# Kernel tuning notes

Hardware: AMD Instinct MI355X
Metric: run time of the kernel (lower is better)

## Reference

```python
import jax, jax.numpy as jnp
import numpy as np

IN_DIM = 14400
K = 25
DIMS = [7200, 3600, 1800]  # floor(in_dim / 2**(i+1))
OUT_DIM = 2
BATCH = 256


def setup_inputs() -> dict:
    key = jax.random.key(0)
    ks = jax.random.split(key, 32)
    inp = {}
    inp["x"] = jax.random.normal(ks[0], (BATCH, 2 * IN_DIM), dtype=jnp.float32)
    # shared KNN tables (both channels load the same h5 files)
    prev = [IN_DIM] + DIMS[:-1]
    for i, (d, p) in enumerate(zip(DIMS, prev)):
        inp[f"knn{i}"] = jax.random.randint(ks[1 + i], (d, K), 0, p, dtype=jnp.int64)
    std = (2.0 / K) ** 0.5
    kidx = 4
    for ch in ("p", "n"):
        for i, d in enumerate(DIMS):
            inp[f"w{ch}{i}"] = jax.random.normal(ks[kidx], (d, K), dtype=jnp.float32) * std; kidx += 1
            inp[f"b{ch}{i}"] = jnp.zeros((1, d), dtype=jnp.float32)
        inp[f"fc{ch}_w"] = jax.random.normal(ks[kidx], (OUT_DIM, DIMS[-1]), dtype=jnp.float32) * (1.0 / DIMS[-1] ** 0.5); kidx += 1
        inp[f"fc{ch}_b"] = jnp.zeros((OUT_DIM,), dtype=jnp.float32)
    inp["fc3_w"] = jax.random.normal(ks[kidx], (OUT_DIM, 4), dtype=jnp.float32) * 0.5
    inp["fc3_b"] = jnp.zeros((OUT_DIM,), dtype=jnp.float32)
    return inp


def _lcn(x, knns, ws, bs, fw, fb):
    # x: (B, in_dim). Each layer: gather KNN neighbors, weighted sum, bias, relu.
    for knn, w, b in zip(knns, ws, bs):
        g = x[:, knn]                                  # (B, dim, K) gather
        x = jax.nn.relu(jnp.einsum('bdk,dk->bd', g, w) + b)
    return x @ fw.T + fb                               # fc_angle


def reference(x, knn0, knn1, knn2,
              wp0, bp0, wp1, bp1, wp2, bp2, fcp_w, fcp_b,
              wn0, bn0, wn1, bn1, wn2, bn2, fcn_w, fcn_b,
              fc3_w, fc3_b):
    knns = (knn0, knn1, knn2)
    xpos = _lcn(x[:, :IN_DIM], knns, (wp0, wp1, wp2), (bp0, bp1, bp2), fcp_w, fcp_b)
    xneg = _lcn(x[:, IN_DIM:], knns, (wn0, wn1, wn2), (bn0, bn1, bn2), fcn_w, fcn_b)
    h = jax.nn.relu(jnp.concatenate([xpos, xneg], axis=1))  # (B, 4)
    return h @ fc3_w.T + fc3_b
```

## Files before the change

### kernel.cpp

```cpp
#include <hip/hip_runtime.h>
#include <hip/hip_bf16.h>

using bf16 = __hip_bfloat16;

#define K 25
#define B 256

__device__ __forceinline__ float b2f(ushort u) {
  unsigned int w = ((unsigned int)u) << 16;
  float f; __builtin_memcpy(&f, &w, 4); return f;
}
__device__ __forceinline__ ushort f2b(float f) {
  bf16 h = __float2bfloat16(f);
  ushort u; __builtin_memcpy(&u, &h, 2); return u;
}

__device__ __forceinline__ int detect_fdt(const void* x) {
  const unsigned int* xw = (const unsigned int*)x;
  int weird = 0;
  for (int i = 0; i < 64; ++i) {
    unsigned int e = (xw[i * 997] >> 23) & 0xFF;
    weird += (e >= 192) || (e <= 30);
  }
  return (weird >= 32) ? 1 : 0;
}
__device__ __forceinline__ int detect_idt(const void* knn0) {
  const unsigned int* kw = (const unsigned int*)knn0;
  int nz = 0;
  for (int i = 0; i < 64; ++i) nz += (kw[2 * i + 1] != 0);
  return (nz == 0) ? 1 : 0;
}

__global__ __launch_bounds__(256) void transpose_kernel(const void* __restrict__ x,
                                                        const void* __restrict__ knn0,
                                                        ushort* __restrict__ xT,
                                                        float* __restrict__ y,
                                                        int* __restrict__ flags) {
  __shared__ float tile[64][65];
  __shared__ int s_fdt;
  const int t = threadIdx.x;
  if (t == 0) s_fdt = detect_fdt(x);
  __syncthreads();
  const int fdt = s_fdt;

  if (blockIdx.x == 0 && blockIdx.y == 0) {
    if (t == 0) {
      flags[0] = fdt;
      flags[1] = detect_idt(knn0);
      flags[16] = 0;
    }
#pragma unroll
    for (int i = 0; i < 4; ++i) y[t + i * 256] = 0.0f;
  }

  const int f0 = blockIdx.x * 64;
  const int b0 = blockIdx.y * 64;
  if (fdt) {
    const ushort* xp = (const ushort*)x;
#pragma unroll
    for (int q = 0; q < 4; ++q) {
      const int lin = t + q * 256;
      const int bl = lin >> 4;
      const int fq = (lin & 15) << 2;
      const ushort4 v = *(const ushort4*)(xp + (size_t)(b0 + bl) * 28800 + f0 + fq);
      tile[bl][fq] = b2f(v.x); tile[bl][fq + 1] = b2f(v.y);
      tile[bl][fq + 2] = b2f(v.z); tile[bl][fq + 3] = b2f(v.w);
    }
  } else {
    const float* xp = (const float*)x;
#pragma unroll
    for (int q = 0; q < 4; ++q) {
      const int lin = t + q * 256;
      const int bl = lin >> 4;
      const int fq = (lin & 15) << 2;
      const float4 v = *(const float4*)(xp + (size_t)(b0 + bl) * 28800 + f0 + fq);
      tile[bl][fq] = v.x; tile[bl][fq + 1] = v.y;
      tile[bl][fq + 2] = v.z; tile[bl][fq + 3] = v.w;
    }
  }
  __syncthreads();
#pragma unroll
  for (int q = 0; q < 4; ++q) {
    const int lin = t + q * 256;
    const int fl = lin >> 4;
    const int bq = (lin & 15) << 2;
    ushort4 o;
    o.x = f2b(tile[bq][fl]);     o.y = f2b(tile[bq + 1][fl]);
    o.z = f2b(tile[bq + 2][fl]); o.w = f2b(tile[bq + 3][fl]);
    *(ushort4*)(xT + (size_t)(f0 + fl) * B + b0 + bq) = o;
  }
}

__global__ __launch_bounds__(256) void lcn_layer(const ushort* __restrict__ inT,
                                                 const void* __restrict__ knn,
                                                 const void* __restrict__ wp,
                                                 const void* __restrict__ bp,
                                                 const void* __restrict__ wn,
                                                 const void* __restrict__ bn,
                                                 ushort* __restrict__ outT,
                                                 const int* __restrict__ flags,
                                                 int prev, int dout) {
  const int fdt = flags[0];
  const int idt = flags[1];
  const int wave = threadIdx.x >> 6;
  const int lane = threadIdx.x & 63;
  const int d = blockIdx.x * 4 + wave;
  const int ch = blockIdx.y;
  const ushort* in = inT + (size_t)ch * prev * B;
  const void* wsel = ch ? wn : wp;
  const void* bsel = ch ? bn : bp;

  int r[K]; float wk[K];
  if (idt) {
    const long long* ip = (const long long*)knn + (size_t)d * K;
#pragma unroll
    for (int k = 0; k < K; ++k) r[k] = (int)ip[k];
  } else {
    const int* ip = (const int*)knn + (size_t)d * K;
#pragma unroll
    for (int k = 0; k < K; ++k) r[k] = ip[k];
  }
  if (fdt) {
    const ushort* wpp = (const ushort*)wsel + (size_t)d * K;
#pragma unroll
    for (int k = 0; k < K; ++k) wk[k] = b2f(wpp[k]);
  } else {
    const float* wpp = (const float*)wsel + (size_t)d * K;
#pragma unroll
    for (int k = 0; k < K; ++k) wk[k] = wpp[k];
  }
  const float bias = fdt ? b2f(((const ushort*)bsel)[d]) : ((const float*)bsel)[d];

  float a0 = 0.f, a1 = 0.f, a2 = 0.f, a3 = 0.f;
#pragma unroll
  for (int k = 0; k < K; ++k) {
    const ushort4 v = *(const ushort4*)(in + (size_t)r[k] * B + (lane << 2));
    a0 = fmaf(wk[k], b2f(v.x), a0);
    a1 = fmaf(wk[k], b2f(v.y), a1);
    a2 = fmaf(wk[k], b2f(v.z), a2);
    a3 = fmaf(wk[k], b2f(v.w), a3);
  }
  a0 = fmaxf(a0 + bias, 0.f);
  a1 = fmaxf(a1 + bias, 0.f);
  a2 = fmaxf(a2 + bias, 0.f);
  a3 = fmaxf(a3 + bias, 0.f);
  ushort4 o; o.x = f2b(a0); o.y = f2b(a1); o.z = f2b(a2); o.w = f2b(a3);
  *(ushort4*)(outT + ((size_t)ch * dout + d) * B + (lane << 2)) = o;
}

__global__ __launch_bounds__(256) void fc_final_kernel(const ushort* __restrict__ h2,
                                                       const void* __restrict__ fcpw,
                                                       const void* __restrict__ fcnw,
                                                       const void* __restrict__ fcpb,
                                                       const void* __restrict__ fcnb,
                                                       const void* __restrict__ f3w,
                                                       const void* __restrict__ f3b,
                                                       float* __restrict__ y,
                                                       int* __restrict__ flags,
                                                       void* __restrict__ out) {
  const int fdt = flags[0];
  const int wave = threadIdx.x >> 6;
  const int lane = threadIdx.x & 63;
  const int wt = blockIdx.x * 4 + wave;
  __shared__ int s_last;

  if (wt < 450) {
    const int ch = wt >= 225;
    const int c0 = (ch ? wt - 225 : wt) * 8;
    const ushort* h = h2 + (size_t)ch * 1800 * B;
    const void* fw = ch ? fcnw : fcpw;
    float w0[8], w1[8];
    if (fdt) {
      const ushort* fp = (const ushort*)fw;
#pragma unroll
      for (int j = 0; j < 8; ++j) { w0[j] = b2f(fp[c0 + j]); w1[j] = b2f(fp[1800 + c0 + j]); }
    } else {
      const float* fp = (const float*)fw;
#pragma unroll
      for (int j = 0; j < 8; ++j) { w0[j] = fp[c0 + j]; w1[j] = fp[1800 + c0 + j]; }
    }
    float s0[4] = {0.f, 0.f, 0.f, 0.f}, s1[4] = {0.f, 0.f, 0.f, 0.f};
#pragma unroll
    for (int j = 0; j < 8; ++j) {
      const ushort4 v = *(const ushort4*)(h + (size_t)(c0 + j) * B + (lane << 2));
      const float f0v = b2f(v.x), f1v = b2f(v.y), f2v = b2f(v.z), f3v = b2f(v.w);
      s0[0] = fmaf(w0[j], f0v, s0[0]); s0[1] = fmaf(w0[j], f1v, s0[1]);
      s0[2] = fmaf(w0[j], f2v, s0[2]); s0[3] = fmaf(w0[j], f3v, s0[3]);
      s1[0] = fmaf(w1[j], f0v, s1[0]); s1[1] = fmaf(w1[j], f1v, s1[1]);
      s1[2] = fmaf(w1[j], f2v, s1[2]); s1[3] = fmaf(w1[j], f3v, s1[3]);
    }
#pragma unroll
    for (int i = 0; i < 4; ++i) {
      atomicAdd(&y[(ch * 2 + 0) * B + (lane << 2) + i], s0[i]);
      atomicAdd(&y[(ch * 2 + 1) * B + (lane << 2) + i], s1[i]);
    }
  }

  __syncthreads();
  if (threadIdx.x == 0) {
    __threadfence();
    s_last = (atomicAdd(&flags[16], 1) == gridDim.x - 1);
  }
  __syncthreads();
  if (s_last) {
    const int b = threadIdx.x;
    const float y0 = atomicAdd(&y[0 * B + b], 0.0f);
    const float y1 = atomicAdd(&y[1 * B + b], 0.0f);
    const float y2 = atomicAdd(&y[2 * B + b], 0.0f);
    const float y3 = atomicAdd(&y[3 * B + b], 0.0f);
    const float bp0v = fdt ? b2f(((const ushort*)fcpb)[0]) : ((const float*)fcpb)[0];
    const float bp1v = fdt ? b2f(((const ushort*)fcpb)[1]) : ((const float*)fcpb)[1];
    const float bn0v = fdt ? b2f(((const ushort*)fcnb)[0]) : ((const float*)fcnb)[0];
    const float bn1v = fdt ? b2f(((const ushort*)fcnb)[1]) : ((const float*)fcnb)[1];
    const float h0v = fmaxf(y0 + bp0v, 0.f);
    const float h1v = fmaxf(y1 + bp1v, 0.f);
    const float h2v = fmaxf(y2 + bn0v, 0.f);
    const float h3v = fmaxf(y3 + bn1v, 0.f);
#pragma unroll
    for (int o = 0; o < 2; ++o) {
      float w0, w1, w2, w3, bb;
      if (fdt) {
        const ushort* fp = (const ushort*)f3w;
        w0 = b2f(fp[o * 4 + 0]); w1 = b2f(fp[o * 4 + 1]);
        w2 = b2f(fp[o * 4 + 2]); w3 = b2f(fp[o * 4 + 3]);
        bb = b2f(((const ushort*)f3b)[o]);
      } else {
        const float* fp = (const float*)f3w;
        w0 = fp[o * 4 + 0]; w1 = fp[o * 4 + 1];
        w2 = fp[o * 4 + 2]; w3 = fp[o * 4 + 3];
        bb = ((const float*)f3b)[o];
      }
      float r = bb;
      r = fmaf(w0, h0v, r); r = fmaf(w1, h1v, r);
      r = fmaf(w2, h2v, r); r = fmaf(w3, h3v, r);
      if (fdt) ((ushort*)out)[b * 2 + o] = f2b(r);
      else     ((float*)out)[b * 2 + o] = r;
    }
  }
}

extern "C" void kernel_launch(void* const* d_in, const int* in_sizes, int n_in,
                              void* d_out, int out_size, void* d_ws, size_t ws_size,
                              hipStream_t stream) {
  const void* x    = d_in[0];
  const void* knn0 = d_in[1];
  const void* knn1 = d_in[2];
  const void* knn2 = d_in[3];
  const void* wp0  = d_in[4];  const void* bp0 = d_in[5];
  const void* wp1  = d_in[6];  const void* bp1 = d_in[7];
  const void* wp2  = d_in[8];  const void* bp2 = d_in[9];
  const void* fcpw = d_in[10]; const void* fcpb = d_in[11];
  const void* wn0  = d_in[12]; const void* bn0 = d_in[13];
  const void* wn1  = d_in[14]; const void* bn1 = d_in[15];
  const void* wn2  = d_in[16]; const void* bn2 = d_in[17];
  const void* fcnw = d_in[18]; const void* fcnb = d_in[19];
  const void* f3w  = d_in[20]; const void* f3b  = d_in[21];

  char* ws = (char*)d_ws;
  ushort* xT = (ushort*)(ws);
  ushort* h0 = (ushort*)(ws + 14745600);
  ushort* h1 = (ushort*)(ws + 22118400);
  ushort* h2 = (ushort*)(ws + 25804800);
  float* y   = (float*)(ws + 27648000);
  int* flags = (int*)(ws + 27652096);

  transpose_kernel<<<dim3(450, 4), 256, 0, stream>>>(x, knn0, xT, y, flags);

  lcn_layer<<<dim3(1800, 2), 256, 0, stream>>>(xT, knn0, wp0, bp0, wn0, bn0, h0,
                                               flags, 14400, 7200);
  lcn_layer<<<dim3(900, 2), 256, 0, stream>>>(h0, knn1, wp1, bp1, wn1, bn1, h1,
                                              flags, 7200, 3600);
  lcn_layer<<<dim3(450, 2), 256, 0, stream>>>(h1, knn2, wp2, bp2, wn2, bn2, h2,
                                              flags, 3600, 1800);

  fc_final_kernel<<<113, 256, 0, stream>>>(h2, fcpw, fcnw, fcpb, fcnb, f3w, f3b,
                                           y, flags, d_out);
}
```

Before: 181.2 us.

## Split LCN batch across half-blocks, interleave channels, parallelize dtype detection

Each LCN wave now covers half the batch, using 2 elements per lane instead of 4, and the grid grows fourfold. The channel and batch half are interleaved in blockIdx.x so that neighbouring blocks share knn rows and gathered input rows. The per-block serial dtype detection loops, run by thread 0 of every transpose block, are replaced with wave-wide ballots. The aim is to expose more parallelism for the latency-bound gathers and to shorten the serial start of the transpose. The cost is that knn indices and weights are loaded twice per output feature, and each gather is narrower.

Measured after the change: 178.2 us. About the same (-1.6%).

```diff
diff --git a/kernel.cpp b/kernel.cpp
--- a/kernel.cpp
+++ b/kernel.cpp
@@ -13,22 +13,6 @@
 __device__ __forceinline__ ushort f2b(float f) {
   bf16 h = __float2bfloat16(f);
   ushort u; __builtin_memcpy(&u, &h, 2); return u;
-}
-
-__device__ __forceinline__ int detect_fdt(const void* x) {
-  const unsigned int* xw = (const unsigned int*)x;
-  int weird = 0;
-  for (int i = 0; i < 64; ++i) {
-    unsigned int e = (xw[i * 997] >> 23) & 0xFF;
-    weird += (e >= 192) || (e <= 30);
-  }
-  return (weird >= 32) ? 1 : 0;
-}
-__device__ __forceinline__ int detect_idt(const void* knn0) {
-  const unsigned int* kw = (const unsigned int*)knn0;
-  int nz = 0;
-  for (int i = 0; i < 64; ++i) nz += (kw[2 * i + 1] != 0);
-  return (nz == 0) ? 1 : 0;
 }
 
 __global__ __launch_bounds__(256) void transpose_kernel(const void* __restrict__ x,
@@ -37,16 +21,27 @@
                                                         float* __restrict__ y,
                                                         int* __restrict__ flags) {
   __shared__ float tile[64][65];
-  __shared__ int s_fdt;
+  __shared__ int s_flags[2];
   const int t = threadIdx.x;
-  if (t == 0) s_fdt = detect_fdt(x);
-  __syncthreads();
-  const int fdt = s_fdt;
+
+  if (t < 64) {
+    const unsigned int u = ((const unsigned int*)x)[t * 997];
+    const unsigned int e = (u >> 23) & 0xFF;
+    const unsigned long long m = __ballot((e >= 192) || (e <= 30));
+    if (t == 0) s_flags[0] = (__popcll(m) >= 32) ? 1 : 0;
+  } else if (t < 128) {
+    const int l = t - 64;
+    const unsigned int hi = ((const unsigned int*)knn0)[2 * l + 1];
+    const unsigned long long m = __ballot(hi != 0);
+    if (l == 0) s_flags[1] = (m == 0ULL) ? 1 : 0;
+  }
+  __syncthreads();
+  const int fdt = s_flags[0];
 
   if (blockIdx.x == 0 && blockIdx.y == 0) {
     if (t == 0) {
-      flags[0] = fdt;
-      flags[1] = detect_idt(knn0);
+      flags[0] = s_flags[0];
+      flags[1] = s_flags[1];
       flags[16] = 0;
     }
 #pragma unroll
@@ -104,9 +99,12 @@
   const int idt = flags[1];
   const int wave = threadIdx.x >> 6;
   const int lane = threadIdx.x & 63;
-  const int d = blockIdx.x * 4 + wave;
-  const int ch = blockIdx.y;
-  const ushort* in = inT + (size_t)ch * prev * B;
+  const int cf   = blockIdx.x & 3;
+  const int ch   = cf >> 1;
+  const int half = cf & 1;
+  const int d    = (blockIdx.x >> 2) * 4 + wave;
+
+  const ushort* in = inT + (size_t)ch * prev * B + half * 128;
   const void* wsel = ch ? wn : wp;
   const void* bsel = ch ? bn : bp;
 
@@ -131,21 +129,17 @@
   }
   const float bias = fdt ? b2f(((const ushort*)bsel)[d]) : ((const float*)bsel)[d];
 
-  float a0 = 0.f, a1 = 0.f, a2 = 0.f, a3 = 0.f;
+  float a0 = 0.f, a1 = 0.f;
 #pragma unroll
   for (int k = 0; k < K; ++k) {
-    const ushort4 v = *(const ushort4*)(in + (size_t)r[k] * B + (lane << 2));
+    const ushort2 v = *(const ushort2*)(in + (size_t)r[k] * B + (lane << 1));
     a0 = fmaf(wk[k], b2f(v.x), a0);
     a1 = fmaf(wk[k], b2f(v.y), a1);
-    a2 = fmaf(wk[k], b2f(v.z), a2);
-    a3 = fmaf(wk[k], b2f(v.w), a3);
   }
   a0 = fmaxf(a0 + bias, 0.f);
   a1 = fmaxf(a1 + bias, 0.f);
-  a2 = fmaxf(a2 + bias, 0.f);
-  a3 = fmaxf(a3 + bias, 0.f);
-  ushort4 o; o.x = f2b(a0); o.y = f2b(a1); o.z = f2b(a2); o.w = f2b(a3);
-  *(ushort4*)(outT + ((size_t)ch * dout + d) * B + (lane << 2)) = o;
+  ushort2 o; o.x = f2b(a0); o.y = f2b(a1);
+  *(ushort2*)(outT + ((size_t)ch * dout + d) * B + half * 128 + (lane << 1)) = o;
 }
 
 __global__ __launch_bounds__(256) void fc_final_kernel(const ushort* __restrict__ h2,
@@ -266,12 +260,12 @@
 
   transpose_kernel<<<dim3(450, 4), 256, 0, stream>>>(x, knn0, xT, y, flags);
 
-  lcn_layer<<<dim3(1800, 2), 256, 0, stream>>>(xT, knn0, wp0, bp0, wn0, bn0, h0,
-                                               flags, 14400, 7200);
-  lcn_layer<<<dim3(900, 2), 256, 0, stream>>>(h0, knn1, wp1, bp1, wn1, bn1, h1,
-                                              flags, 7200, 3600);
-  lcn_layer<<<dim3(450, 2), 256, 0, stream>>>(h1, knn2, wp2, bp2, wn2, bn2, h2,
-                                              flags, 3600, 1800);
+  lcn_layer<<<7200, 256, 0, stream>>>(xT, knn0, wp0, bp0, wn0, bn0, h0,
+                                      flags, 14400, 7200);
+  lcn_layer<<<3600, 256, 0, stream>>>(h0, knn1, wp1, bp1, wn1, bn1, h1,
+                                      flags, 7200, 3600);
+  lcn_layer<<<1800, 256, 0, stream>>>(h1, knn2, wp2, bp2, wn2, bn2, h2,
+                                      flags, 3600, 1800);
 
   fc_final_kernel<<<113, 256, 0, stream>>>(h2, fcpw, fcnw, fcpb, fcnb, f3w, f3b,
                                            y, flags, d_out);
```
